# Kernel tuning notes

Measured on AMD Instinct MI355X. Metric: run time of the kernel, lower is better.

## Reference

```python
import jax, jax.numpy as jnp
import numpy as np

N_SEG, N_REG, N_EDGE, HID, CHEB_K = 40000, 1000, 640000, 256, 5


def setup_inputs() -> dict:
    key = jax.random.key(0)
    ks = jax.random.split(key, 6)
    return {
        "projected_region_features": jax.random.normal(ks[0], (N_REG, HID), jnp.float32),
        "segment2region_assignment": jax.random.uniform(ks[1], (N_SEG, N_REG), jnp.float32),
        "edge_index": jax.random.randint(ks[2], (2, N_EDGE), 0, N_SEG, dtype=jnp.int64),
        # ChebConv params: one [HID,HID] weight per Chebyshev order + shared bias
        "cheb_W": jax.random.normal(ks[3], (CHEB_K, HID, HID), jnp.float32) / np.sqrt(HID).astype(np.float32),
        "cheb_b": jnp.zeros((HID,), jnp.float32),
        "ln_gamma": jnp.ones((HID,), jnp.float32),
        "ln_beta": jnp.zeros((HID,), jnp.float32),
    }


def _cheb_conv(x, edge_index, W, b):
    """PyG ChebConv with normalization='sym', lambda_max=2.0.
    Scaled Laplacian L_hat = 2L/lam - I = -D^{-1/2} A D^{-1/2} (diag = 0)."""
    N = x.shape[0]
    src, dst = edge_index[0], edge_index[1]
    w = (src != dst).astype(x.dtype)  # remove_self_loops
    deg = jax.ops.segment_sum(w, src, num_segments=N)
    dinv = jnp.where(deg > 0, jax.lax.rsqrt(jnp.where(deg > 0, deg, 1.0)), 0.0)
    norm = -w * dinv[src] * dinv[dst]  # per-edge weight of L_hat

    def prop(t):  # y_i = sum_{(j->i)} norm_e * t_j
        return jax.ops.segment_sum(norm[:, None] * t[src], dst, num_segments=N)

    Tx0 = x
    out = Tx0 @ W[0]
    Tx1 = prop(Tx0)
    out = out + Tx1 @ W[1]
    for k in range(2, W.shape[0]):
        Tx2 = 2.0 * prop(Tx1) - Tx0
        out = out + Tx2 @ W[k]
        Tx0, Tx1 = Tx1, Tx2
    return out + b


def _layer_norm(x, g, b, eps=1e-5):
    mu = jnp.mean(x, axis=-1, keepdims=True)
    var = jnp.mean(jnp.square(x - mu), axis=-1, keepdims=True)
    return (x - mu) * jax.lax.rsqrt(var + eps) * g + b


def reference(projected_region_features, segment2region_assignment, edge_index,
              cheb_W, cheb_b, ln_gamma, ln_beta):
    # [n_seg, n_reg] @ [n_reg, hid] -> [n_seg, hid]
    seg_low_raw = segment2region_assignment @ projected_region_features
    seg_low = _cheb_conv(seg_low_raw, edge_index, cheb_W, cheb_b)
    seg_low = _layer_norm(jax.nn.gelu(seg_low, approximate=False), ln_gamma, ln_beta)
    return (seg_low, seg_low_raw)
```

## Files before the change

### kernel.cpp

```cpp
#include <hip/hip_runtime.h>

#define NSEG 40000
#define NREG 1000
#define NEDGE 640000
#define HID 256
#define KCAT 1280
#define KP1 1024
#define LPAD 40
#define NBLK 157

typedef float f32x4 __attribute__((ext_vector_type(4)));
typedef short s16x8 __attribute__((ext_vector_type(8)));
typedef unsigned short u16x4 __attribute__((ext_vector_type(4)));
typedef unsigned short u16x8 __attribute__((ext_vector_type(8)));

typedef __attribute__((address_space(3))) unsigned int lds_u32;
typedef __attribute__((address_space(1))) const unsigned int glb_u32;

__device__ __forceinline__ void dma16(const void* g, void* l) {
    __builtin_amdgcn_global_load_lds((glb_u32*)g, (lds_u32*)l, 16, 0, 0);
}

__device__ __forceinline__ unsigned short f2bf(float f) {
    unsigned u = __builtin_bit_cast(unsigned, f);
    u += 0x7FFFu + ((u >> 16) & 1u);
    return (unsigned short)(u >> 16);
}
__device__ __forceinline__ float bf2f(unsigned short h) {
    unsigned u = ((unsigned)h) << 16;
    return __builtin_bit_cast(float, u);
}

__device__ __forceinline__ f32x4 mfma16(s16x8 a, s16x8 b, f32x4 c) {
    return __builtin_amdgcn_mfma_f32_16x16x32_bf16(a, b, c, 0, 0, 0);
}

__global__ void detect_kernel(const unsigned int* __restrict__ E, int* flag) {
    int lane = threadIdx.x;
    unsigned v = E[2 * lane + 1];
    unsigned long long m = __ballot(v == 0u);
    if (lane == 0) *flag = (__popcll(m) >= 48) ? 1 : 0;
}

__device__ __forceinline__ int edge_at(const void* E, int idx, int is64) {
    return is64 ? (int)((const long long*)E)[idx] : ((const int*)E)[idx];
}

__global__ __launch_bounds__(256) void deg_cnt_kernel(const void* __restrict__ E,
                                                      const int* __restrict__ flag,
                                                      int* deg, int* cnt) {
    int e = blockIdx.x * 256 + threadIdx.x;
    if (e >= NEDGE) return;
    int is64 = *flag;
    int s = edge_at(E, e, is64);
    int d = edge_at(E, e + NEDGE, is64);
    if (s != d) {
        atomicAdd(&deg[s], 1);
        atomicAdd(&cnt[d], 1);
    }
}

__global__ __launch_bounds__(256) void dinv_kernel(const int* __restrict__ deg,
                                                   float* __restrict__ dinv) {
    int i = blockIdx.x * 256 + threadIdx.x;
    if (i < NSEG) {
        int d = deg[i];
        dinv[i] = d > 0 ? rsqrtf((float)d) : 0.f;
    }
}

__global__ __launch_bounds__(256) void scan1_kernel(const int* __restrict__ cnt,
                                                    int* __restrict__ bsum) {
    __shared__ int sh[256];
    int t = threadIdx.x;
    int i = blockIdx.x * 256 + t;
    sh[t] = (i < NSEG) ? cnt[i] : 0;
    __syncthreads();
    for (int o = 128; o > 0; o >>= 1) {
        if (t < o) sh[t] += sh[t + o];
        __syncthreads();
    }
    if (t == 0) bsum[blockIdx.x] = sh[0];
}

__global__ __launch_bounds__(256) void scan2_kernel(const int* __restrict__ bsum,
                                                    int* __restrict__ boff,
                                                    int* __restrict__ rowptr) {
    __shared__ int sh[256];
    int t = threadIdx.x;
    int v = (t < NBLK) ? bsum[t] : 0;
    sh[t] = v;
    __syncthreads();
    for (int o = 1; o < 256; o <<= 1) {
        int x = 0;
        if (t >= o) x = sh[t - o];
        __syncthreads();
        if (t >= o) sh[t] += x;
        __syncthreads();
    }
    if (t < NBLK) boff[t] = sh[t] - v;
    if (t == 255) rowptr[NSEG] = sh[255];
}

__global__ __launch_bounds__(256) void scan3_kernel(const int* __restrict__ cnt,
                                                    const int* __restrict__ boff,
                                                    int* __restrict__ rowptr,
                                                    int* __restrict__ cursor) {
    __shared__ int sh[256];
    int t = threadIdx.x;
    int i = blockIdx.x * 256 + t;
    int v = (i < NSEG) ? cnt[i] : 0;
    sh[t] = v;
    __syncthreads();
    for (int o = 1; o < 256; o <<= 1) {
        int x = 0;
        if (t >= o) x = sh[t - o];
        __syncthreads();
        if (t >= o) sh[t] += x;
        __syncthreads();
    }
    if (i < NSEG) {
        int p = boff[blockIdx.x] + sh[t] - v;
        rowptr[i] = p;
        cursor[i] = p;
    }
}

__global__ __launch_bounds__(256) void scatter_kernel(const void* __restrict__ E,
                                                      const int* __restrict__ flag,
                                                      const float* __restrict__ dinv,
                                                      int* cursor,
                                                      long long* __restrict__ colval) {
    int e = blockIdx.x * 256 + threadIdx.x;
    if (e >= NEDGE) return;
    int is64 = *flag;
    int s = edge_at(E, e, is64);
    int d = edge_at(E, e + NEDGE, is64);
    if (s != d) {
        int pos = atomicAdd(&cursor[d], 1);
        float v = -dinv[s] * dinv[d];
        colval[pos] = ((long long)(unsigned)__builtin_bit_cast(unsigned, v) << 32)
                    | (unsigned)s;
    }
}

__global__ void prep_w_kernel(const float* __restrict__ P, const float* __restrict__ W,
                              unsigned short* __restrict__ Pt, unsigned short* __restrict__ Wt) {
    int n = blockIdx.x;
    for (int k = threadIdx.x; k < KP1; k += blockDim.x)
        Pt[(size_t)n * KP1 + k] = (k < NREG) ? f2bf(P[(size_t)k * HID + n]) : (unsigned short)0;
    for (int k = threadIdx.x; k < KCAT; k += blockDim.x)
        Wt[(size_t)n * KCAT + k] = f2bf(W[(size_t)k * HID + n]);
}

__global__ __launch_bounds__(256) void gemm1_kernel(const float* __restrict__ S,
                                                    const unsigned short* __restrict__ Pt,
                                                    float* __restrict__ raw,
                                                    unsigned short* __restrict__ xcat) {
    __shared__ unsigned short As[64][LPAD];
    __shared__ unsigned short Bs[256][LPAD];
    const int m0 = blockIdx.x * 64;
    const int tid = threadIdx.x;
    const int lane = tid & 63, wn = tid >> 6;
    const int r = lane & 15, q = lane >> 4;
    const int srow = tid >> 2, scol = (tid & 3) * 8;

    f32x4 acc[4][4] = {};

    for (int kb = 0; kb < NREG; kb += 32) {
        const bool kvalid = (kb + scol + 8 <= NREG);
        u16x8 av = {0, 0, 0, 0, 0, 0, 0, 0};
        u16x8 bv0 = av, bv1 = av, bv2 = av, bv3 = av;
        if (kvalid) {
            const float* sp = S + (size_t)(m0 + srow) * NREG + kb + scol;
            f32x4 f0 = *(const f32x4*)sp;
            f32x4 f1 = *(const f32x4*)(sp + 4);
            av[0] = f2bf(f0[0]); av[1] = f2bf(f0[1]); av[2] = f2bf(f0[2]); av[3] = f2bf(f0[3]);
            av[4] = f2bf(f1[0]); av[5] = f2bf(f1[1]); av[6] = f2bf(f1[2]); av[7] = f2bf(f1[3]);
            bv0 = *(const u16x8*)(Pt + (size_t)(srow)       * KP1 + kb + scol);
            bv1 = *(const u16x8*)(Pt + (size_t)(srow +  64) * KP1 + kb + scol);
            bv2 = *(const u16x8*)(Pt + (size_t)(srow + 128) * KP1 + kb + scol);
            bv3 = *(const u16x8*)(Pt + (size_t)(srow + 192) * KP1 + kb + scol);
        }
        __syncthreads();
        *(u16x8*)&As[srow][scol] = av;
        *(u16x8*)&Bs[srow][scol] = bv0;
        *(u16x8*)&Bs[srow + 64][scol] = bv1;
        *(u16x8*)&Bs[srow + 128][scol] = bv2;
        *(u16x8*)&Bs[srow + 192][scol] = bv3;
        __syncthreads();
        s16x8 af[4], bfv[4];
#pragma unroll
        for (int am = 0; am < 4; ++am) af[am] = *(const s16x8*)&As[am * 16 + r][q * 8];
#pragma unroll
        for (int bn = 0; bn < 4; ++bn) bfv[bn] = *(const s16x8*)&Bs[wn * 64 + bn * 16 + r][q * 8];
#pragma unroll
        for (int am = 0; am < 4; ++am) {
#pragma unroll
            for (int bn = 0; bn < 4; ++bn)
                acc[am][bn] = mfma16(af[am], bfv[bn], acc[am][bn]);
        }
    }
#pragma unroll
    for (int am = 0; am < 4; ++am) {
        int rowb = m0 + am * 16 + q * 4;
#pragma unroll
        for (int bn = 0; bn < 4; ++bn) {
            int col = wn * 64 + bn * 16 + r;
#pragma unroll
            for (int i = 0; i < 4; ++i) {
                float v = acc[am][bn][i];
                raw[(size_t)(rowb + i) * HID + col] = v;
                xcat[(size_t)(rowb + i) * KCAT + col] = f2bf(v);
            }
        }
    }
}

__global__ __launch_bounds__(256) void prop_kernel(unsigned short* xcat,
                                                   const int* __restrict__ rowptr,
                                                   const long long* __restrict__ colval,
                                                   int inOff, int outOff, int subOff,
                                                   float scale) {
    const int g = blockIdx.x * 4 + (threadIdx.x >> 6);
    const int lane = threadIdx.x & 63;
    const int half = lane >> 5;
    const int l5 = lane & 31;
    const int e0 = rowptr[g], e1 = rowptr[g + 1];
    float a0 = 0.f, a1 = 0.f, a2 = 0.f, a3 = 0.f;
    float a4 = 0.f, a5 = 0.f, a6 = 0.f, a7 = 0.f;
    const unsigned short* xin = xcat + inOff + l5 * 8;

    for (int base = e0; base < e1; base += 64) {
        int m = e1 - base;
        if (m > 64) m = 64;
        int cc = 0;
        float vv = 0.f;
        if (lane < m) {
            long long cv = colval[base + lane];
            cc = (int)(unsigned)cv;
            vv = __builtin_bit_cast(float, (unsigned)(cv >> 32));
        }
        int i = 0;
#pragma unroll 4
        for (; i + 2 <= m; i += 2) {
            int c = __shfl(cc, i + half);
            float v = __shfl(vv, i + half);
            u16x8 t = *(const u16x8*)(xin + (size_t)c * KCAT);
            a0 += v * bf2f(t[0]); a1 += v * bf2f(t[1]);
            a2 += v * bf2f(t[2]); a3 += v * bf2f(t[3]);
            a4 += v * bf2f(t[4]); a5 += v * bf2f(t[5]);
            a6 += v * bf2f(t[6]); a7 += v * bf2f(t[7]);
        }
        if (i < m) {
            int c = __shfl(cc, i);
            float v = __shfl(vv, i);
            if (half == 0) {
                u16x8 t = *(const u16x8*)(xin + (size_t)c * KCAT);
                a0 += v * bf2f(t[0]); a1 += v * bf2f(t[1]);
                a2 += v * bf2f(t[2]); a3 += v * bf2f(t[3]);
                a4 += v * bf2f(t[4]); a5 += v * bf2f(t[5]);
                a6 += v * bf2f(t[6]); a7 += v * bf2f(t[7]);
            }
        }
    }
    a0 += __shfl_xor(a0, 32); a1 += __shfl_xor(a1, 32);
    a2 += __shfl_xor(a2, 32); a3 += __shfl_xor(a3, 32);
    a4 += __shfl_xor(a4, 32); a5 += __shfl_xor(a5, 32);
    a6 += __shfl_xor(a6, 32); a7 += __shfl_xor(a7, 32);

    if (half == 0) {
        a0 *= scale; a1 *= scale; a2 *= scale; a3 *= scale;
        a4 *= scale; a5 *= scale; a6 *= scale; a7 *= scale;
        if (subOff >= 0) {
            u16x8 p = *(const u16x8*)(xcat + (size_t)g * KCAT + subOff + l5 * 8);
            a0 -= bf2f(p[0]); a1 -= bf2f(p[1]); a2 -= bf2f(p[2]); a3 -= bf2f(p[3]);
            a4 -= bf2f(p[4]); a5 -= bf2f(p[5]); a6 -= bf2f(p[6]); a7 -= bf2f(p[7]);
        }
        u16x8 o = {f2bf(a0), f2bf(a1), f2bf(a2), f2bf(a3),
                   f2bf(a4), f2bf(a5), f2bf(a6), f2bf(a7)};
        *(u16x8*)(xcat + (size_t)g * KCAT + outOff + l5 * 8) = o;
    }
}

__global__ __launch_bounds__(512) void gemm2_kernel(const unsigned short* __restrict__ xcat,
                                                    const unsigned short* __restrict__ Wt,
                                                    const float* __restrict__ bias,
                                                    const float* __restrict__ gamma,
                                                    const float* __restrict__ beta,
                                                    float* __restrict__ outp) {
    __shared__ unsigned short As[2][128 * 32];
    __shared__ unsigned short Bs[2][256 * 32];
    __shared__ float rs[128][4];
    __shared__ float rss[128][4];
    const int tid = threadIdx.x;
    const int lane = tid & 63, wid = tid >> 6;
    const int wm = wid >> 2, wn = wid & 3;
    const int r = lane & 15, q = lane >> 4;
    const int qx8 = (q ^ (r & 3)) << 3;
    const int m0 = blockIdx.x * 128;
    const int crow = lane >> 2;
    const int bcol = (((lane & 3) ^ ((lane >> 2) & 3)) << 3);

    f32x4 acc[4][4] = {};

    auto stage = [&](int c, int kb) {
#pragma unroll
        for (int k = 0; k < 3; ++k) {
            int idx = 3 * wid + k;
            if (idx < 16) {
                int n = idx * 16 + crow;
                dma16(Wt + (size_t)n * KCAT + kb + bcol, &Bs[c][idx * 512]);
            } else {
                int a = idx - 16;
                int row = m0 + a * 16 + crow;
                dma16(xcat + (size_t)row * KCAT + kb + bcol, &As[c][a * 512]);
            }
        }
    };

    stage(0, 0);
    __syncthreads();

    for (int t = 0; t < 40; ++t) {
        const int c = t & 1;
        if (t < 39) stage(c ^ 1, (t + 1) * 32);
        s16x8 af[4], bfv[4];
#pragma unroll
        for (int am = 0; am < 4; ++am)
            af[am] = *(const s16x8*)&As[c][(wm * 64 + am * 16 + r) * 32 + qx8];
#pragma unroll
        for (int bn = 0; bn < 4; ++bn)
            bfv[bn] = *(const s16x8*)&Bs[c][(wn * 64 + bn * 16 + r) * 32 + qx8];
#pragma unroll
        for (int am = 0; am < 4; ++am)
#pragma unroll
            for (int bn = 0; bn < 4; ++bn)
                acc[am][bn] = mfma16(af[am], bfv[bn], acc[am][bn]);
        __syncthreads();
    }

    float bc[4], gm[4], bt[4];
#pragma unroll
    for (int bn = 0; bn < 4; ++bn) {
        int col = wn * 64 + bn * 16 + r;
        bc[bn] = bias[col];
        gm[bn] = gamma[col];
        bt[bn] = beta[col];
    }
#pragma unroll
    for (int am = 0; am < 4; ++am) {
#pragma unroll
        for (int i = 0; i < 4; ++i) {
            float s = 0.f, ss = 0.f;
#pragma unroll
            for (int bn = 0; bn < 4; ++bn) {
                float v = acc[am][bn][i] + bc[bn];
                v = 0.5f * v * (1.f + erff(v * 0.70710678118654752f));
                acc[am][bn][i] = v;
                s += v;
                ss += v * v;
            }
#pragma unroll
            for (int msk = 1; msk < 16; msk <<= 1) {
                s += __shfl_xor(s, msk);
                ss += __shfl_xor(ss, msk);
            }
            if (r == 0) {
                int row = wm * 64 + am * 16 + q * 4 + i;
                rs[row][wn] = s;
                rss[row][wn] = ss;
            }
        }
    }
    __syncthreads();
#pragma unroll
    for (int am = 0; am < 4; ++am) {
#pragma unroll
        for (int i = 0; i < 4; ++i) {
            int row = wm * 64 + am * 16 + q * 4 + i;
            float s = rs[row][0] + rs[row][1] + rs[row][2] + rs[row][3];
            float ss = rss[row][0] + rss[row][1] + rss[row][2] + rss[row][3];
            float mu = s * (1.f / HID);
            float var = ss * (1.f / HID) - mu * mu;
            float inv = rsqrtf(var + 1e-5f);
            if (m0 + row < NSEG) {
#pragma unroll
                for (int bn = 0; bn < 4; ++bn) {
                    int col = wn * 64 + bn * 16 + r;
                    outp[(size_t)(m0 + row) * HID + col] = (acc[am][bn][i] - mu) * inv * gm[bn] + bt[bn];
                }
            }
        }
    }
}

extern "C" void kernel_launch(void* const* d_in, const int* in_sizes, int n_in,
                              void* d_out, int out_size, void* d_ws, size_t ws_size,
                              hipStream_t stream) {
    const float* P     = (const float*)d_in[0];
    const float* S     = (const float*)d_in[1];
    const void*  E     = d_in[2];
    const float* W     = (const float*)d_in[3];
    const float* bias  = (const float*)d_in[4];
    const float* gamma = (const float*)d_in[5];
    const float* beta  = (const float*)d_in[6];

    float* out = (float*)d_out;
    float* raw = out + (size_t)NSEG * HID;

    char* ws = (char*)d_ws;
    size_t off = 0;
    auto alloc = [&](size_t bytes) -> void* {
        void* p = ws + off;
        off += (bytes + 255) & ~(size_t)255;
        return p;
    };
    unsigned short* xcat   = (unsigned short*)alloc((size_t)NSEG * KCAT * 2);
    unsigned short* Pt     = (unsigned short*)alloc((size_t)HID * KP1 * 2);
    unsigned short* Wt     = (unsigned short*)alloc((size_t)HID * KCAT * 2);
    int*            deg    = (int*)alloc((size_t)NSEG * 4);
    float*          dinv   = (float*)alloc((size_t)NSEG * 4);
    int*            cnt    = (int*)alloc((size_t)NSEG * 4);
    int*            rowptr = (int*)alloc((size_t)(NSEG + 1) * 4);
    int*            cursor = (int*)alloc((size_t)NSEG * 4);
    long long*      colval = (long long*)alloc((size_t)NEDGE * 8);
    int*            bsum   = (int*)alloc((size_t)NBLK * 4);
    int*            boff   = (int*)alloc((size_t)NBLK * 4);
    int*            flag   = (int*)alloc(256);
    if (off > ws_size) return;

    hipMemsetAsync(deg, 0, (size_t)NSEG * 4, stream);
    hipMemsetAsync(cnt, 0, (size_t)NSEG * 4, stream);

    detect_kernel<<<1, 64, 0, stream>>>((const unsigned int*)E, flag);
    prep_w_kernel<<<HID, 256, 0, stream>>>(P, W, Pt, Wt);

    deg_cnt_kernel<<<NEDGE / 256, 256, 0, stream>>>(E, flag, deg, cnt);
    dinv_kernel<<<(NSEG + 255) / 256, 256, 0, stream>>>(deg, dinv);
    scan1_kernel<<<NBLK, 256, 0, stream>>>(cnt, bsum);
    scan2_kernel<<<1, 256, 0, stream>>>(bsum, boff, rowptr);
    scan3_kernel<<<NBLK, 256, 0, stream>>>(cnt, boff, rowptr, cursor);
    scatter_kernel<<<NEDGE / 256, 256, 0, stream>>>(E, flag, dinv, cursor, colval);

    gemm1_kernel<<<NSEG / 64, 256, 0, stream>>>(S, Pt, raw, xcat);

    prop_kernel<<<NSEG / 4, 256, 0, stream>>>(xcat, rowptr, colval, 0 * HID, 1 * HID, -1, 1.f);
    prop_kernel<<<NSEG / 4, 256, 0, stream>>>(xcat, rowptr, colval, 1 * HID, 2 * HID, 0 * HID, 2.f);
    prop_kernel<<<NSEG / 4, 256, 0, stream>>>(xcat, rowptr, colval, 2 * HID, 3 * HID, 1 * HID, 2.f);
    prop_kernel<<<NSEG / 4, 256, 0, stream>>>(xcat, rowptr, colval, 3 * HID, 4 * HID, 2 * HID, 2.f);

    gemm2_kernel<<<(NSEG + 127) / 128, 512, 0, stream>>>(xcat, Wt, bias, gamma, beta, out);
}
```

Measured before the change: 431.5 us.

## Gather FP8 copies of Chebyshev features in sparse propagation, fuse dinv into scan

Adds an FP8 shadow copy of the feature concat buffer, written by gemm1 and by each propagation step except the last. The sparse propagation kernels now gather 8-byte FP8 rows instead of 16-byte bf16 rows, which halves the random-gather traffic that dominates the prop kernels. The bf16 outputs are still written for the final GEMM. Separately, the dinv computation is folded into scan1 to save one launch. FP8 (e4m3) gathers lose precision and may break accuracy tolerance, and the extra byte writes add some store traffic. The gemm1 FP8 writes are scattered single bytes.

```diff
diff --git a/kernel.cpp b/kernel.cpp
--- a/kernel.cpp
+++ b/kernel.cpp
@@ -10,9 +10,11 @@
 #define NBLK 157
 
 typedef float f32x4 __attribute__((ext_vector_type(4)));
+typedef float f32x2 __attribute__((ext_vector_type(2)));
 typedef short s16x8 __attribute__((ext_vector_type(8)));
 typedef unsigned short u16x4 __attribute__((ext_vector_type(4)));
 typedef unsigned short u16x8 __attribute__((ext_vector_type(8)));
+typedef unsigned int u32x2 __attribute__((ext_vector_type(2)));
 
 typedef __attribute__((address_space(3))) unsigned int lds_u32;
 typedef __attribute__((address_space(1))) const unsigned int glb_u32;
@@ -29,6 +31,9 @@
 __device__ __forceinline__ float bf2f(unsigned short h) {
     unsigned u = ((unsigned)h) << 16;
     return __builtin_bit_cast(float, u);
+}
+__device__ __forceinline__ unsigned char f2fp8(float v) {
+    return (unsigned char)__builtin_amdgcn_cvt_pk_fp8_f32(v, v, 0, false);
 }
 
 __device__ __forceinline__ f32x4 mfma16(s16x8 a, s16x8 b, f32x4 c) {
@@ -60,21 +65,19 @@
     }
 }
 
-__global__ __launch_bounds__(256) void dinv_kernel(const int* __restrict__ deg,
-                                                   float* __restrict__ dinv) {
-    int i = blockIdx.x * 256 + threadIdx.x;
-    if (i < NSEG) {
-        int d = deg[i];
-        dinv[i] = d > 0 ? rsqrtf((float)d) : 0.f;
-    }
-}
-
 __global__ __launch_bounds__(256) void scan1_kernel(const int* __restrict__ cnt,
+                                                    const int* __restrict__ deg,
+                                                    float* __restrict__ dinv,
                                                     int* __restrict__ bsum) {
     __shared__ int sh[256];
     int t = threadIdx.x;
     int i = blockIdx.x * 256 + t;
-    sh[t] = (i < NSEG) ? cnt[i] : 0;
+    int c = (i < NSEG) ? cnt[i] : 0;
+    sh[t] = c;
+    if (i < NSEG) {
+        int d = deg[i];
+        dinv[i] = d > 0 ? rsqrtf((float)d) : 0.f;
+    }
     __syncthreads();
     for (int o = 128; o > 0; o >>= 1) {
         if (t < o) sh[t] += sh[t + o];
@@ -156,7 +159,8 @@
 __global__ __launch_bounds__(256) void gemm1_kernel(const float* __restrict__ S,
                                                     const unsigned short* __restrict__ Pt,
                                                     float* __restrict__ raw,
-                                                    unsigned short* __restrict__ xcat) {
+                                                    unsigned short* __restrict__ xcat,
+                                                    unsigned char* __restrict__ x8) {
     __shared__ unsigned short As[64][LPAD];
     __shared__ unsigned short Bs[256][LPAD];
     const int m0 = blockIdx.x * 64;
@@ -212,16 +216,18 @@
                 float v = acc[am][bn][i];
                 raw[(size_t)(rowb + i) * HID + col] = v;
                 xcat[(size_t)(rowb + i) * KCAT + col] = f2bf(v);
+                x8[(size_t)(rowb + i) * KCAT + col] = f2fp8(v);
             }
         }
     }
 }
 
 __global__ __launch_bounds__(256) void prop_kernel(unsigned short* xcat,
+                                                   unsigned char* x8,
                                                    const int* __restrict__ rowptr,
                                                    const long long* __restrict__ colval,
                                                    int inOff, int outOff, int subOff,
-                                                   float scale) {
+                                                   float scale, int writeFp8) {
     const int g = blockIdx.x * 4 + (threadIdx.x >> 6);
     const int lane = threadIdx.x & 63;
     const int half = lane >> 5;
@@ -229,7 +235,7 @@
     const int e0 = rowptr[g], e1 = rowptr[g + 1];
     float a0 = 0.f, a1 = 0.f, a2 = 0.f, a3 = 0.f;
     float a4 = 0.f, a5 = 0.f, a6 = 0.f, a7 = 0.f;
-    const unsigned short* xin = xcat + inOff + l5 * 8;
+    const unsigned char* xin = x8 + inOff + l5 * 8;
 
     for (int base = e0; base < e1; base += 64) {
         int m = e1 - base;
@@ -246,21 +252,29 @@
         for (; i + 2 <= m; i += 2) {
             int c = __shfl(cc, i + half);
             float v = __shfl(vv, i + half);
-            u16x8 t = *(const u16x8*)(xin + (size_t)c * KCAT);
-            a0 += v * bf2f(t[0]); a1 += v * bf2f(t[1]);
-            a2 += v * bf2f(t[2]); a3 += v * bf2f(t[3]);
-            a4 += v * bf2f(t[4]); a5 += v * bf2f(t[5]);
-            a6 += v * bf2f(t[6]); a7 += v * bf2f(t[7]);
+            u32x2 t = *(const u32x2*)(xin + (size_t)c * KCAT);
+            f32x2 d0 = __builtin_amdgcn_cvt_pk_f32_fp8(t[0], false);
+            f32x2 d1 = __builtin_amdgcn_cvt_pk_f32_fp8(t[0], true);
+            f32x2 d2 = __builtin_amdgcn_cvt_pk_f32_fp8(t[1], false);
+            f32x2 d3 = __builtin_amdgcn_cvt_pk_f32_fp8(t[1], true);
+            a0 += v * d0[0]; a1 += v * d0[1];
+            a2 += v * d1[0]; a3 += v * d1[1];
+            a4 += v * d2[0]; a5 += v * d2[1];
+            a6 += v * d3[0]; a7 += v * d3[1];
         }
         if (i < m) {
             int c = __shfl(cc, i);
             float v = __shfl(vv, i);
             if (half == 0) {
-                u16x8 t = *(const u16x8*)(xin + (size_t)c * KCAT);
-                a0 += v * bf2f(t[0]); a1 += v * bf2f(t[1]);
-                a2 += v * bf2f(t[2]); a3 += v * bf2f(t[3]);
-                a4 += v * bf2f(t[4]); a5 += v * bf2f(t[5]);
-                a6 += v * bf2f(t[6]); a7 += v * bf2f(t[7]);
+                u32x2 t = *(const u32x2*)(xin + (size_t)c * KCAT);
+                f32x2 d0 = __builtin_amdgcn_cvt_pk_f32_fp8(t[0], false);
+                f32x2 d1 = __builtin_amdgcn_cvt_pk_f32_fp8(t[0], true);
+                f32x2 d2 = __builtin_amdgcn_cvt_pk_f32_fp8(t[1], false);
+                f32x2 d3 = __builtin_amdgcn_cvt_pk_f32_fp8(t[1], true);
+                a0 += v * d0[0]; a1 += v * d0[1];
+                a2 += v * d1[0]; a3 += v * d1[1];
+                a4 += v * d2[0]; a5 += v * d2[1];
+                a6 += v * d3[0]; a7 += v * d3[1];
             }
         }
     }
@@ -280,6 +294,15 @@
         u16x8 o = {f2bf(a0), f2bf(a1), f2bf(a2), f2bf(a3),
                    f2bf(a4), f2bf(a5), f2bf(a6), f2bf(a7)};
         *(u16x8*)(xcat + (size_t)g * KCAT + outOff + l5 * 8) = o;
+        if (writeFp8) {
+            unsigned p0 = 0, p1 = 0;
+            p0 = __builtin_amdgcn_cvt_pk_fp8_f32(a0, a1, (int)p0, false);
+            p0 = __builtin_amdgcn_cvt_pk_fp8_f32(a2, a3, (int)p0, true);
+            p1 = __builtin_amdgcn_cvt_pk_fp8_f32(a4, a5, (int)p1, false);
+            p1 = __builtin_amdgcn_cvt_pk_fp8_f32(a6, a7, (int)p1, true);
+            u32x2 o8 = {p0, p1};
+            *(u32x2*)(x8 + (size_t)g * KCAT + outOff + l5 * 8) = o8;
+        }
     }
 }
 
@@ -417,6 +440,7 @@
         return p;
     };
     unsigned short* xcat   = (unsigned short*)alloc((size_t)NSEG * KCAT * 2);
+    unsigned char*  x8     = (unsigned char*)alloc((size_t)NSEG * KCAT);
     unsigned short* Pt     = (unsigned short*)alloc((size_t)HID * KP1 * 2);
     unsigned short* Wt     = (unsigned short*)alloc((size_t)HID * KCAT * 2);
     int*            deg    = (int*)alloc((size_t)NSEG * 4);
@@ -437,18 +461,17 @@
     prep_w_kernel<<<HID, 256, 0, stream>>>(P, W, Pt, Wt);
 
     deg_cnt_kernel<<<NEDGE / 256, 256, 0, stream>>>(E, flag, deg, cnt);
-    dinv_kernel<<<(NSEG + 255) / 256, 256, 0, stream>>>(deg, dinv);
-    scan1_kernel<<<NBLK, 256, 0, stream>>>(cnt, bsum);
+    scan1_kernel<<<NBLK, 256, 0, stream>>>(cnt, deg, dinv, bsum);
     scan2_kernel<<<1, 256, 0, stream>>>(bsum, boff, rowptr);
     scan3_kernel<<<NBLK, 256, 0, stream>>>(cnt, boff, rowptr, cursor);
     scatter_kernel<<<NEDGE / 256, 256, 0, stream>>>(E, flag, dinv, cursor, colval);
 
-    gemm1_kernel<<<NSEG / 64, 256, 0, stream>>>(S, Pt, raw, xcat);
-
-    prop_kernel<<<NSEG / 4, 256, 0, stream>>>(xcat, rowptr, colval, 0 * HID, 1 * HID, -1, 1.f);
-    prop_kernel<<<NSEG / 4, 256, 0, stream>>>(xcat, rowptr, colval, 1 * HID, 2 * HID, 0 * HID, 2.f);
-    prop_kernel<<<NSEG / 4, 256, 0, stream>>>(xcat, rowptr, colval, 2 * HID, 3 * HID, 1 * HID, 2.f);
-    prop_kernel<<<NSEG / 4, 256, 0, stream>>>(xcat, rowptr, colval, 3 * HID, 4 * HID, 2 * HID, 2.f);
+    gemm1_kernel<<<NSEG / 64, 256, 0, stream>>>(S, Pt, raw, xcat, x8);
+
+    prop_kernel<<<NSEG / 4, 256, 0, stream>>>(xcat, x8, rowptr, colval, 0 * HID, 1 * HID, -1, 1.f, 1);
+    prop_kernel<<<NSEG / 4, 256, 0, stream>>>(xcat, x8, rowptr, colval, 1 * HID, 2 * HID, 0 * HID, 2.f, 1);
+    prop_kernel<<<NSEG / 4, 256, 0, stream>>>(xcat, x8, rowptr, colval, 2 * HID, 3 * HID, 1 * HID, 2.f, 1);
+    prop_kernel<<<NSEG / 4, 256, 0, stream>>>(xcat, x8, rowptr, colval, 3 * HID, 4 * HID, 2 * HID, 2.f, 0);
 
     gemm2_kernel<<<(NSEG + 127) / 128, 512, 0, stream>>>(xcat, Wt, bias, gamma, beta, out);
 }
```

After: 385.5 us. 1.12x faster.
